# Kernel tuning notes

Hardware: AMD Instinct MI355X
Metric: run time of the kernel (lower is better)

## Reference

```python
import jax, jax.numpy as jnp
import numpy as np

B, N, M, T, D, NH = 64, 1024, 32, 8, 512, 8
OUT = 1000
NSO, NSA = N // 4, N // 8
DH = D // NH


def _conv(x, w, b):
    y = jax.lax.conv_general_dilated(x, w, (1, 1), 'SAME', dimension_numbers=('NCHW', 'OIHW', 'NCHW'))
    return y + b[None, :, None, None]


def _bn(x, g, b):
    # BatchNorm2d in train mode: per-batch statistics over (B, H, W)
    m = x.mean(axis=(0, 2, 3), keepdims=True)
    v = x.var(axis=(0, 2, 3), keepdims=True)
    return (x - m) * jax.lax.rsqrt(v + 1e-5) * g[None, :, None, None] + b[None, :, None, None]


def _mp2(x):
    b_, c, h, w = x.shape
    return x.reshape(b_, c, h // 2, 2, w // 2, 2).max(axis=(3, 5))


def _ln(x, g, b):
    m = x.mean(-1, keepdims=True)
    v = x.var(-1, keepdims=True)
    return (x - m) * jax.lax.rsqrt(v + 1e-5) * g + b


def _glu(x):
    a, b = jnp.split(x, 2, axis=-1)
    return a * jax.nn.sigmoid(b)


def setup_inputs():
    ks = iter(jax.random.split(jax.random.key(0), 64))

    def nrm(shape, fan_in):
        return jax.random.normal(next(ks), shape, jnp.float32) / np.float32(np.sqrt(fan_in))

    inp = {}
    inp['x'] = jax.random.normal(next(ks), (B, 3, 64, 64), jnp.float32)
    inp['c1w'] = nrm((16, 3, 3, 3), 27); inp['c1b'] = jnp.zeros((16,))
    inp['bn1g'] = jnp.ones((16,)); inp['bn1b'] = jnp.zeros((16,))
    inp['c2w'] = nrm((32, 16, 3, 3), 144); inp['c2b'] = jnp.zeros((32,))
    inp['bn2g'] = jnp.ones((32,)); inp['bn2b'] = jnp.zeros((32,))
    inp['c3w'] = nrm((64, 32, 3, 3), 288); inp['c3b'] = jnp.zeros((64,))
    inp['bn3g'] = jnp.ones((64,)); inp['bn3b'] = jnp.zeros((64,))
    inp['c4w'] = nrm((64, 64, 3, 3), 576); inp['c4b'] = jnp.zeros((64,))
    inp['bn4g'] = jnp.ones((64,)); inp['bn4b'] = jnp.zeros((64,))
    inp['fc1w'] = nrm((256, 256), 256); inp['fc1b'] = jnp.zeros((256,))
    inp['fc2w'] = nrm((128, D), 128); inp['fc2b'] = jnp.zeros((D,))
    inp['kvw'] = nrm((D, D), D); inp['kvb'] = jnp.zeros((D,))
    inp['kvlg'] = jnp.ones((D,)); inp['kvlb'] = jnp.zeros((D,))
    inp['synw'] = nrm((D + N, 2 * N), D + N); inp['synb'] = jnp.zeros((2 * N,))
    inp['synlg'] = jnp.ones((N,)); inp['synlb'] = jnp.zeros((N,))
    inp['nlm_w1'] = nrm((N, M, 256), M); inp['nlm_b1'] = jnp.zeros((N, 256))
    inp['nlm_w2'] = nrm((N, 128), 128); inp['nlm_b2'] = jnp.zeros((N,))
    inp['start_act'] = nrm((N,), N)
    inp['start_trace'] = nrm((N, M), N + M)
    inp['dec_a'] = jax.random.uniform(next(ks), (NSA,), jnp.float32, 0.0, 3.0)
    inp['dec_o'] = jax.random.uniform(next(ks), (NSO,), jnp.float32, 0.0, 3.0)
    inp['qw'] = nrm((NSA, D), NSA); inp['qb'] = jnp.zeros((D,))
    inp['attn_inw'] = nrm((D, 3 * D), D); inp['attn_inb'] = jnp.zeros((3 * D,))
    inp['attn_ow'] = nrm((D, D), D); inp['attn_ob'] = jnp.zeros((D,))
    inp['op_w1'] = nrm((NSO, 256), NSO); inp['op_b1'] = jnp.zeros((256,))
    inp['op_l1g'] = jnp.ones((256,)); inp['op_l1b'] = jnp.zeros((256,))
    inp['op_w2'] = nrm((256, 64), 256); inp['op_b2'] = jnp.zeros((64,))
    inp['op_l2g'] = jnp.ones((64,)); inp['op_l2b'] = jnp.zeros((64,))
    inp['op_w3'] = nrm((64, OUT), 64); inp['op_b3'] = jnp.zeros((OUT,))
    inp['aL'] = jax.random.randint(next(ks), (NSA,), 0, N)
    inp['aR'] = jax.random.randint(next(ks), (NSA,), 0, N)
    inp['oL'] = jax.random.randint(next(ks), (NSO,), 0, N)
    inp['oR'] = jax.random.randint(next(ks), (NSO,), 0, N)
    inp['task_idx'] = 0
    return inp


def _forward(x, c1w, c1b, bn1g, bn1b, c2w, c2b, bn2g, bn2b, c3w, c3b, bn3g, bn3b, c4w, c4b, bn4g, bn4b, fc1w, fc1b, fc2w, fc2b, kvw, kvb, kvlg, kvlb, synw, synb, synlg, synlb, nlm_w1, nlm_b1, nlm_w2, nlm_b2, start_act, start_trace, dec_a, dec_o, qw, qb, attn_inw, attn_inb, attn_ow, attn_ob, op_w1, op_b1, op_l1g, op_l1b, op_w2, op_b2, op_l2g, op_l2b, op_w3, op_b3, aL, aR, oL, oR):
    # --- AdaptiveCNNEncoder (3-channel branch) ---
    h = jax.nn.relu(_bn(_conv(x, c1w, c1b), bn1g, bn1b))
    h = jax.nn.relu(_bn(_conv(h, c2w, c2b), bn2g, bn2b))
    h = _mp2(h)
    h = jax.nn.relu(_bn(_conv(h, c3w, c3b), bn3g, bn3b))
    h = _mp2(h)
    h = jax.nn.relu(_bn(_conv(h, c4w, c4b), bn4g, bn4b))
    b_, c, hh, ww = h.shape
    # AdaptiveAvgPool2d((2,2)): mean over equal blocks (16x16 -> 2x2)
    h = h.reshape(b_, c, 2, hh // 2, 2, ww // 2).mean(axis=(3, 5)).reshape(b_, c * 4)
    enc = _glu(h @ fc1w + fc1b) @ fc2w + fc2b            # (B, D)
    kv = _ln(enc @ kvw + kvb, kvlg, kvlb)                # single kv token

    Wq, Wk, Wv = jnp.split(attn_inw, 3, axis=1)
    bq, bk, bv = jnp.split(attn_inb, 3)
    kh = (kv @ Wk + bk).reshape(B, NH, DH)
    vh = (kv @ Wv + bv).reshape(B, NH, DH)

    r_a = jnp.exp(-jnp.clip(dec_a, 0.0, 15.0))           # (NSA,)
    r_o = jnp.exp(-jnp.clip(dec_o, 0.0, 15.0))           # (NSO,)

    act0 = jnp.broadcast_to(start_act, (B, N))
    trace0 = jnp.broadcast_to(start_trace, (B, N, M))
    ao0 = act0[:, oL] * act0[:, oR]                      # initial out-sync accumulators
    bo0 = jnp.ones_like(ao0)
    inv_log_out = np.float32(1.0 / np.log(OUT))
    inv_sqrt_dh = np.float32(1.0 / np.sqrt(DH))

    def tick(carry, t):
        act, trace, aa, ba, ao, bo = carry
        pp = act[:, aL] * act[:, aR]
        first = (t == 0)
        aa = jnp.where(first, pp, r_a * aa + pp)
        ba = jnp.where(first, jnp.ones_like(ba), r_a * ba + 1.0)
        sync_a = aa * jax.lax.rsqrt(ba + 1e-8)
        qv = sync_a @ qw + qb
        qh = (qv @ Wq + bq).reshape(B, NH, DH)
        logits = jnp.einsum('bhd,bhd->bh', qh, kh) * inv_sqrt_dh
        w = jax.nn.softmax(logits[..., None], axis=-1)[..., 0]  # single key -> ones
        attn_out = (w[..., None] * vh).reshape(B, D) @ attn_ow + attn_ob
        pre = jnp.concatenate([attn_out, act], axis=-1)
        state = _ln(_glu(pre @ synw + synb), synlg, synlb)
        trace = jnp.concatenate([trace[:, :, 1:], state[:, :, None]], axis=-1)
        # per-neuron private MLPs, batched: (B,N,M)x(N,M,256) -> GLU -> (N,128) -> scalar
        hid = _glu(jnp.einsum('bnm,nmh->bnh', trace, nlm_w1) + nlm_b1)
        act = jnp.einsum('bnh,nh->bn', hid, nlm_w2) + nlm_b2
        po = act[:, oL] * act[:, oR]
        ao = r_o * ao + po
        bo = r_o * bo + 1.0
        sync_o = ao * jax.lax.rsqrt(bo + 1e-8)
        h1 = jax.nn.relu(_ln(sync_o @ op_w1 + op_b1, op_l1g, op_l1b))
        h2 = jax.nn.relu(_ln(h1 @ op_w2 + op_b2, op_l2g, op_l2b))
        pred = h2 @ op_w3 + op_b3
        p = jax.nn.softmax(pred, axis=-1)
        ent = -jnp.sum(p * jnp.log(p + 1e-10), axis=-1)
        ne = ent * inv_log_out
        cert = jnp.stack([ne, 1.0 - ne], axis=-1)
        return (act, trace, aa, ba, ao, bo), (pred, cert)

    carry0 = (act0, trace0, jnp.zeros((B, NSA), jnp.float32), jnp.zeros((B, NSA), jnp.float32), ao0, bo0)
    _, (preds, certs) = jax.lax.scan(tick, carry0, jnp.arange(T))
    return jnp.transpose(preds, (1, 2, 0)), jnp.transpose(certs, (1, 2, 0))


def reference(x, c1w, c1b, bn1g, bn1b, c2w, c2b, bn2g, bn2b, c3w, c3b, bn3g, bn3b, c4w, c4b, bn4g, bn4b, fc1w, fc1b, fc2w, fc2b, kvw, kvb, kvlg, kvlb, synw, synb, synlg, synlb, nlm_w1, nlm_b1, nlm_w2, nlm_b2, start_act, start_trace, dec_a, dec_o, qw, qb, attn_inw, attn_inb, attn_ow, attn_ob, op_w1, op_b1, op_l1g, op_l1b, op_w2, op_b2, op_l2g, op_l2b, op_w3, op_b3, aL, aR, oL, oR, task_idx):
    del task_idx  # single task; all task-indexed params are for task 0
    return _forward(x, c1w, c1b, bn1g, bn1b, c2w, c2b, bn2g, bn2b, c3w, c3b, bn3g, bn3b, c4w, c4b, bn4g, bn4b, fc1w, fc1b, fc2w, fc2b, kvw, kvb, kvlg, kvlb, synw, synb, synlg, synlb, nlm_w1, nlm_b1, nlm_w2, nlm_b2, start_act, start_trace, dec_a, dec_o, qw, qb, attn_inw, attn_inb, attn_ow, attn_ob, op_w1, op_b1, op_l1g, op_l1b, op_w2, op_b2, op_l2g, op_l2b, op_w3, op_b3, aL, aR, oL, oR)
```

## Files before the change

kernel.cpp:

```cpp
#include <hip/hip_runtime.h>
#include <math.h>

constexpr int B_ = 64, N_ = 1024, M_ = 32, T_ = 8;
constexpr int OUT_ = 1000, NSO_ = 256;

#define DEVFN __device__ __forceinline__

typedef __attribute__((ext_vector_type(8))) short bf16x8;
typedef __attribute__((ext_vector_type(4))) float f32x4;

DEVFN float blockReduceSum(float v, float* buf) {
  int t = threadIdx.x;
  buf[t] = v; __syncthreads();
  for (int off = blockDim.x >> 1; off > 0; off >>= 1) {
    if (t < off) buf[t] += buf[t + off];
    __syncthreads();
  }
  float r = buf[0];
  __syncthreads();
  return r;
}

DEVFN float sigmoidf_(float x) { return 1.f / (1.f + __expf(-x)); }

DEVFN unsigned short f2bf(float f) {
  unsigned u = __float_as_uint(f);
  unsigned r = (u + 0x7FFFu + ((u >> 16) & 1u)) >> 16;
  return (unsigned short)r;
}
DEVFN float bf2f(unsigned short h) { return __uint_as_float((unsigned)h << 16); }

template<int NW>
DEVFN float bsum(float v, float* red) {
  #pragma unroll
  for (int o = 32; o > 0; o >>= 1) v += __shfl_xor(v, o);
  int w = threadIdx.x >> 6, ln = threadIdx.x & 63;
  if (ln == 0) red[w] = v;
  __syncthreads();
  if (w == 0) {
    float x = (ln < NW) ? red[ln] : 0.f;
    #pragma unroll
    for (int o = 8; o > 0; o >>= 1) x += __shfl_xor(x, o);
    if (ln == 0) red[0] = x;
  }
  __syncthreads();
  float r = red[0];
  __syncthreads();
  return r;
}

template<int NW>
DEVFN float bmax(float v, float* red) {
  #pragma unroll
  for (int o = 32; o > 0; o >>= 1) v = fmaxf(v, __shfl_xor(v, o));
  int w = threadIdx.x >> 6, ln = threadIdx.x & 63;
  if (ln == 0) red[w] = v;
  __syncthreads();
  if (w == 0) {
    float x = (ln < NW) ? red[ln] : -INFINITY;
    #pragma unroll
    for (int o = 8; o > 0; o >>= 1) x = fmaxf(x, __shfl_xor(x, o));
    if (ln == 0) red[0] = x;
  }
  __syncthreads();
  float r = red[0];
  __syncthreads();
  return r;
}

DEVFN void bn_ssl(float2* ssl, const float* bnpart, const float* g, const float* bb,
                  int C, int ns, float inv_n) {
  for (int c = threadIdx.x; c < C; c += blockDim.x) {
    float s1 = 0.f, s2 = 0.f;
    for (int s = 0; s < ns; ++s) { s1 += bnpart[(c * ns + s) * 2]; s2 += bnpart[(c * ns + s) * 2 + 1]; }
    float m = s1 * inv_n;
    float var = s2 * inv_n - m * m;
    float rstd = rsqrtf(var + 1e-5f);
    float sc = g[c] * rstd;
    ssl[c] = make_float2(sc, bb[c] - m * sc);
  }
}

__global__ __launch_bounds__(256)
void k_wprep(const float* __restrict__ c2w, const float* __restrict__ c3w,
             const float* __restrict__ c4w, unsigned short* __restrict__ wt2,
             unsigned short* __restrict__ wt3, unsigned short* __restrict__ wt4) {
  int i = blockIdx.x * 256 + threadIdx.x;
  if (i < 5120) {
    int tap = i / 512, co = (i / 16) % 32, ci = i & 15;
    wt2[i] = (tap < 9) ? f2bf(c2w[(co * 16 + ci) * 9 + tap]) : 0;
  } else if (i < 5120 + 18432) {
    int j = i - 5120;
    int tap = j / 2048, co = (j / 32) % 64, ci = j & 31;
    wt3[j] = f2bf(c3w[(co * 32 + ci) * 9 + tap]);
  } else if (i < 5120 + 18432 + 36864) {
    int j = i - 5120 - 18432;
    int tap = j / 4096, co = (j / 64) % 64, ci = j & 63;
    wt4[j] = f2bf(c4w[(co * 64 + ci) * 9 + tap]);
  }
}

__global__ __launch_bounds__(256)
void k_w1t(const float* __restrict__ w1, unsigned short* __restrict__ w1t) {
  int n = blockIdx.x;
  __shared__ float tile[32][260];
  const float* src = w1 + (size_t)n * 8192;
  for (int i = threadIdx.x; i < 8192; i += 256)
    tile[i >> 8][i & 255] = src[i];
  __syncthreads();
  int c = threadIdx.x;
  unsigned short* dst = w1t + ((size_t)n * 256 + c) * 32;
  #pragma unroll
  for (int q = 0; q < 8; ++q) {
    ushort4 o;
    o.x = f2bf(tile[q * 4 + 0][c]); o.y = f2bf(tile[q * 4 + 1][c]);
    o.z = f2bf(tile[q * 4 + 2][c]); o.w = f2bf(tile[q * 4 + 3][c]);
    *reinterpret_cast<ushort4*>(dst + q * 4) = o;
  }
}

__global__ __launch_bounds__(256)
void k_synwt(const float* __restrict__ synw2, unsigned short* __restrict__ Bt) {
  int j0 = blockIdx.x * 64, k0 = blockIdx.y * 64;
  __shared__ float tile[64][65];
  for (int i = threadIdx.x; i < 4096; i += 256) {
    int kk = i >> 6, jj = i & 63;
    tile[kk][jj] = synw2[(size_t)(k0 + kk) * 2048 + j0 + jj];
  }
  __syncthreads();
  int jj = threadIdx.x >> 2, kq = (threadIdx.x & 3) * 16;
  unsigned short* dst = Bt + (size_t)(j0 + jj) * 1024 + k0 + kq;
  #pragma unroll
  for (int q = 0; q < 4; ++q) {
    ushort4 o;
    o.x = f2bf(tile[kq + q * 4 + 0][jj]); o.y = f2bf(tile[kq + q * 4 + 1][jj]);
    o.z = f2bf(tile[kq + q * 4 + 2][jj]); o.w = f2bf(tile[kq + q * 4 + 3][jj]);
    *reinterpret_cast<ushort4*>(dst + q * 4) = o;
  }
}

__global__ __launch_bounds__(256)
void k_conv1(const float* __restrict__ in, const float* __restrict__ wgl,
             unsigned short* __restrict__ outp) {
  constexpr int HW = 64, TY = 4, XV = 4, XQ = 16, CPT = 4;
  __shared__ __align__(16) float ins[3][TY + 2][HW + 8];
  const int b = blockIdx.x, y0 = blockIdx.y * TY, tid = threadIdx.x;
  const int sp = tid & 63;
  const int cg = __builtin_amdgcn_readfirstlane(tid >> 6);
  const int xq = sp % XQ, yr = sp / XQ, x0 = xq * XV;
  float acc[CPT][XV];
  #pragma unroll
  for (int j = 0; j < CPT; ++j)
    #pragma unroll
    for (int k = 0; k < XV; ++k) acc[j][k] = 0.f;
  constexpr int NEL = 3 * (TY + 2) * (HW + 8);
  for (int i = tid; i < NEL; i += 256) {
    int col = i % (HW + 8), row = (i / (HW + 8)) % (TY + 2), ci = i / ((HW + 8) * (TY + 2));
    int gx = col - 4, gy = y0 + row - 1;
    float v = 0.f;
    if (gx >= 0 && gx < HW && gy >= 0 && gy < HW)
      v = in[((size_t)(b * 3 + ci) * HW + gy) * HW + gx];
    ins[ci][row][col] = v;
  }
  __syncthreads();
  for (int ci = 0; ci < 3; ++ci) {
    const float* wci = wgl + ((size_t)(cg * CPT) * 3 + ci) * 9;
    #pragma unroll
    for (int dy = 0; dy < 3; ++dy) {
      const float* r = &ins[ci][yr + dy][x0 + 4];
      float win[6];
      win[0] = r[-1];
      float4 m = *reinterpret_cast<const float4*>(r);
      win[1] = m.x; win[2] = m.y; win[3] = m.z; win[4] = m.w;
      win[5] = r[4];
      #pragma unroll
      for (int j = 0; j < CPT; ++j) {
        const float* wj = wci + (size_t)j * 27 + dy * 3;
        float w0 = wj[0], w1 = wj[1], w2 = wj[2];
        #pragma unroll
        for (int k = 0; k < XV; ++k)
          acc[j][k] = fmaf(win[k], w0, fmaf(win[k + 1], w1, fmaf(win[k + 2], w2, acc[j][k])));
      }
    }
  }
  #pragma unroll
  for (int j = 0; j < CPT; ++j) {
    unsigned short* op = outp + (((size_t)b * 16 + cg * CPT + j) * HW + y0 + yr) * HW + x0;
    ushort4 o;
    o.x = f2bf(acc[j][0]); o.y = f2bf(acc[j][1]); o.z = f2bf(acc[j][2]); o.w = f2bf(acc[j][3]);
    *reinterpret_cast<ushort4*>(op) = o;
  }
}

__global__ __launch_bounds__(256)
void k_conv2_mfma(const unsigned short* __restrict__ in, const unsigned short* __restrict__ wt2,
                  const float* __restrict__ bnpart, const float* __restrict__ bng,
                  const float* __restrict__ bnb, unsigned short* __restrict__ outp) {
  const int b = blockIdx.x, y = blockIdx.y;
  const int tid = threadIdx.x;
  const int w = tid >> 6, lane = tid & 63;
  const int col = lane & 15, kg = lane >> 4;
  const int p0 = w * 16;
  __shared__ unsigned short lds[3][68][16];
  __shared__ float2 ssl[16];
  bn_ssl(ssl, bnpart, bng, bnb, 16, 32, 1.f / (float)(B_ * 4096));
  __syncthreads();
  for (int i = tid; i < 3 * 66 * 16; i += 256) {
    int px = i % 66, row = (i / 66) % 3, ci = i / 198;
    int gy = y + row - 1, gx = px - 1;
    float v = 0.f;
    if (gy >= 0 && gy < 64 && gx >= 0 && gx < 64) {
      float2 s = ssl[ci];
      v = fmaxf(fmaf(bf2f(in[((size_t)(b * 16 + ci) * 64 + gy) * 64 + gx]), s.x, s.y), 0.f);
    }
    lds[row][px][ci] = f2bf(v);
  }
  __syncthreads();
  f32x4 acc0 = {0.f, 0.f, 0.f, 0.f}, acc1 = {0.f, 0.f, 0.f, 0.f};
  const int tsel = kg >> 1, ci0 = (kg & 1) * 8;
  #pragma unroll
  for (int p = 0; p < 5; ++p) {
    int tap = 2 * p + tsel;
    int dy = (tap < 9) ? tap / 3 : 0;
    int dx = (tap < 9) ? tap % 3 : 0;
    bf16x8 af = *reinterpret_cast<const bf16x8*>(&lds[dy][p0 + col + dx][ci0]);
    bf16x8 b0 = *reinterpret_cast<const bf16x8*>(wt2 + ((size_t)tap * 32 + col) * 16 + ci0);
    bf16x8 b1 = *reinterpret_cast<const bf16x8*>(wt2 + ((size_t)tap * 32 + 16 + col) * 16 + ci0);
    acc0 = __builtin_amdgcn_mfma_f32_16x16x32_bf16(af, b0, acc0, 0, 0, 0);
    acc1 = __builtin_amdgcn_mfma_f32_16x16x32_bf16(af, b1, acc1, 0, 0, 0);
  }
  int px = p0 + kg * 4;
  ushort4 o0, o1;
  o0.x = f2bf(acc0[0]); o0.y = f2bf(acc0[1]); o0.z = f2bf(acc0[2]); o0.w = f2bf(acc0[3]);
  o1.x = f2bf(acc1[0]); o1.y = f2bf(acc1[1]); o1.z = f2bf(acc1[2]); o1.w = f2bf(acc1[3]);
  *reinterpret_cast<ushort4*>(outp + ((size_t)(b * 32 + col) * 64 + y) * 64 + px) = o0;
  *reinterpret_cast<ushort4*>(outp + ((size_t)(b * 32 + 16 + col) * 64 + y) * 64 + px) = o1;
}

__global__ __launch_bounds__(256)
void k_conv3_mfma(const unsigned short* __restrict__ in, const unsigned short* __restrict__ wt3,
                  const float* __restrict__ bnpart, const float* __restrict__ bng,
                  const float* __restrict__ bnb, unsigned short* __restrict__ outp) {
  const int b = blockIdx.x, y0 = blockIdx.y * 2;
  const int tid = threadIdx.x;
  const int w = tid >> 6, lane = tid & 63;
  const int col = lane & 15, kg = lane >> 4;
  const int yloc = w >> 1, p0 = (w & 1) * 16;
  __shared__ unsigned short lds[4][34][40];
  __shared__ float2 ssl[32];
  bn_ssl(ssl, bnpart, bng, bnb, 32, 32, 1.f / (float)(B_ * 4096));
  __syncthreads();
  for (int i = tid; i < 4 * 34 * 32; i += 256) {
    int px = i % 34, row = (i / 34) % 4, ci = i / 136;
    int gy = y0 + row - 1, gx = px - 1;
    float v = 0.f;
    if (gy >= 0 && gy < 32 && gx >= 0 && gx < 32) {
      float2 s = ssl[ci];
      size_t base = ((size_t)(b * 32 + ci) * 64 + 2 * gy) * 64 + 2 * gx;
      float r0 = fmaf(bf2f(in[base]),      s.x, s.y);
      float r1 = fmaf(bf2f(in[base + 1]),  s.x, s.y);
      float r2 = fmaf(bf2f(in[base + 64]), s.x, s.y);
      float r3 = fmaf(bf2f(in[base + 65]), s.x, s.y);
      v = fmaxf(fmaxf(fmaxf(r0, r1), fmaxf(r2, r3)), 0.f);
    }
    lds[row][px][ci] = f2bf(v);
  }
  __syncthreads();
  f32x4 acc[4];
  #pragma unroll
  for (int c = 0; c < 4; ++c) acc[c] = (f32x4){0.f, 0.f, 0.f, 0.f};
  #pragma unroll
  for (int tap = 0; tap < 9; ++tap) {
    int dy = tap / 3, dx = tap % 3;
    bf16x8 af = *reinterpret_cast<const bf16x8*>(&lds[yloc + dy][p0 + col + dx][kg * 8]);
    #pragma unroll
    for (int c = 0; c < 4; ++c) {
      bf16x8 bfr = *reinterpret_cast<const bf16x8*>(wt3 + ((size_t)tap * 64 + c * 16 + col) * 32 + kg * 8);
      acc[c] = __builtin_amdgcn_mfma_f32_16x16x32_bf16(af, bfr, acc[c], 0, 0, 0);
    }
  }
  int yy = y0 + yloc, px = p0 + kg * 4;
  #pragma unroll
  for (int c = 0; c < 4; ++c) {
    ushort4 o;
    o.x = f2bf(acc[c][0]); o.y = f2bf(acc[c][1]); o.z = f2bf(acc[c][2]); o.w = f2bf(acc[c][3]);
    *reinterpret_cast<ushort4*>(outp + ((size_t)(b * 64 + c * 16 + col) * 32 + yy) * 32 + px) = o;
  }
}

__global__ __launch_bounds__(128)
void k_conv4_mfma(const unsigned short* __restrict__ in, const unsigned short* __restrict__ wt4,
                  const float* __restrict__ bnpart, const float* __restrict__ bng,
                  const float* __restrict__ bnb, unsigned short* __restrict__ outp) {
  const int b = blockIdx.x, y0 = blockIdx.y * 2;
  const int tid = threadIdx.x;
  const int w = tid >> 6, lane = tid & 63;
  const int col = lane & 15, kg = lane >> 4;
  __shared__ unsigned short lds[4][18][72];
  __shared__ float2 ssl[64];
  bn_ssl(ssl, bnpart, bng, bnb, 64, 16, 1.f / (float)(B_ * 1024));
  __syncthreads();
  for (int i = tid; i < 4 * 18 * 64; i += 128) {
    int px = i % 18, row = (i / 18) % 4, ci = i / 72;
    int gy = y0 + row - 1, gx = px - 1;
    float v = 0.f;
    if (gy >= 0 && gy < 16 && gx >= 0 && gx < 16) {
      float2 s = ssl[ci];
      size_t base = ((size_t)(b * 64 + ci) * 32 + 2 * gy) * 32 + 2 * gx;
      float r0 = fmaf(bf2f(in[base]),      s.x, s.y);
      float r1 = fmaf(bf2f(in[base + 1]),  s.x, s.y);
      float r2 = fmaf(bf2f(in[base + 32]), s.x, s.y);
      float r3 = fmaf(bf2f(in[base + 33]), s.x, s.y);
      v = fmaxf(fmaxf(fmaxf(r0, r1), fmaxf(r2, r3)), 0.f);
    }
    lds[row][px][ci] = f2bf(v);
  }
  __syncthreads();
  f32x4 acc[4];
  #pragma unroll
  for (int c = 0; c < 4; ++c) acc[c] = (f32x4){0.f, 0.f, 0.f, 0.f};
  #pragma unroll
  for (int tap = 0; tap < 9; ++tap) {
    int dy = tap / 3, dx = tap % 3;
    #pragma unroll
    for (int kc = 0; kc < 2; ++kc) {
      bf16x8 af = *reinterpret_cast<const bf16x8*>(&lds[w + dy][col + dx][kc * 32 + kg * 8]);
      #pragma unroll
      for (int c = 0; c < 4; ++c) {
        bf16x8 bfr = *reinterpret_cast<const bf16x8*>(wt4 + ((size_t)tap * 64 + c * 16 + col) * 64 + kc * 32 + kg * 8);
        acc[c] = __builtin_amdgcn_mfma_f32_16x16x32_bf16(af, bfr, acc[c], 0, 0, 0);
      }
    }
  }
  int yy = y0 + w, px = kg * 4;
  #pragma unroll
  for (int c = 0; c < 4; ++c) {
    ushort4 o;
    o.x = f2bf(acc[c][0]); o.y = f2bf(acc[c][1]); o.z = f2bf(acc[c][2]); o.w = f2bf(acc[c][3]);
    *reinterpret_cast<ushort4*>(outp + ((size_t)(b * 64 + c * 16 + col) * 16 + yy) * 16 + px) = o;
  }
}

template<int C, int HW2>
__global__ __launch_bounds__(256)
void k_bn_stats_bf(const unsigned short* __restrict__ x, float* __restrict__ part) {
  int c = blockIdx.x, s = blockIdx.y, ns = gridDim.y;
  const int Np2 = B_ * HW2 / 2;
  float s1 = 0.f, s2 = 0.f;
  for (int ii = s * 256 + threadIdx.x; ii < Np2; ii += ns * 256) {
    int b = ii / (HW2 / 2), p2 = ii % (HW2 / 2);
    const unsigned short* pp = x + ((size_t)b * C + c) * HW2 + p2 * 2;
    unsigned u = *reinterpret_cast<const unsigned*>(pp);
    float v0 = __uint_as_float(u << 16);
    float v1 = __uint_as_float(u & 0xFFFF0000u);
    s1 += v0 + v1; s2 += v0 * v0 + v1 * v1;
  }
  __shared__ float r1[256], r2[256];
  r1[threadIdx.x] = s1; r2[threadIdx.x] = s2; __syncthreads();
  for (int off = 128; off > 0; off >>= 1) {
    if (threadIdx.x < off) { r1[threadIdx.x] += r1[threadIdx.x + off]; r2[threadIdx.x] += r2[threadIdx.x + off]; }
    __syncthreads();
  }
  if (threadIdx.x == 0) {
    part[(c * ns + s) * 2 + 0] = r1[0];
    part[(c * ns + s) * 2 + 1] = r2[0];
  }
}

__global__ __launch_bounds__(256)
void k_avgpool_bn_bf(const unsigned short* __restrict__ x, const float* __restrict__ bnpart,
                     const float* __restrict__ g, const float* __restrict__ bb,
                     float* __restrict__ outp) {
  __shared__ float2 ssl[64];
  bn_ssl(ssl, bnpart, g, bb, 64, 8, 1.f / (float)(B_ * 256));
  __syncthreads();
  int idx = blockIdx.x * 256 + threadIdx.x;
  int b = idx >> 8;
  int r = idx & 255;
  int c = r >> 2, i = (r >> 1) & 1, j = r & 1;
  float2 s = ssl[c];
  const unsigned short* p = x + ((size_t)(b * 64 + c) * 16 + i * 8) * 16 + j * 8;
  float sum = 0.f;
  #pragma unroll
  for (int yy = 0; yy < 8; ++yy)
    #pragma unroll
    for (int xx = 0; xx < 8; ++xx)
      sum += fmaxf(fmaf(bf2f(p[yy * 16 + xx]), s.x, s.y), 0.f);
  outp[idx] = sum * (1.f / 64.f);
}

template<int K, int NOUT>
__global__ __launch_bounds__(256)
void k_gemm_part(const float* __restrict__ A, const float* __restrict__ W, int ldw,
                 float* __restrict__ part) {
  int jt = blockIdx.x, ks = blockIdx.y;
  int k0 = ks * 64;
  __shared__ float As[64][65];
  for (int i = threadIdx.x; i < 4096; i += 256) {
    int r = i >> 6, c = i & 63;
    As[r][c] = A[(size_t)r * K + k0 + c];
  }
  __syncthreads();
  int jsub = threadIdx.x & 31;
  int bg = threadIdx.x >> 5;
  int j = jt * 32 + jsub;
  float acc[8] = {0.f, 0.f, 0.f, 0.f, 0.f, 0.f, 0.f, 0.f};
  const float* wp = W + (size_t)k0 * ldw + j;
  #pragma unroll 8
  for (int kk = 0; kk < 64; ++kk) {
    float w = wp[(size_t)kk * ldw];
    #pragma unroll
    for (int r = 0; r < 8; ++r) acc[r] = fmaf(As[bg * 8 + r][kk], w, acc[r]);
  }
  float* pp = part + (size_t)ks * 64 * NOUT + j;
  #pragma unroll
  for (int r = 0; r < 8; ++r) pp[(size_t)(bg * 8 + r) * NOUT] = acc[r];
}

template<int NOUT, int NO_FIN, int KS, bool GLU_, bool LN_>
__global__ __launch_bounds__(256)
void k_fc_reduce(const float* __restrict__ part, const float* __restrict__ bias, int bstride,
                 const float* __restrict__ lng, const float* __restrict__ lnb,
                 float* __restrict__ outp) {
  constexpr int R = (NO_FIN + 255) / 256;
  int b = blockIdx.x, t = threadIdx.x;
  const float* bp = bias + (size_t)b * bstride;
  float v[R];
  #pragma unroll
  for (int r = 0; r < R; ++r) {
    int j = t + r * 256;
    if (j < NO_FIN) {
      float za = bp[j];
      float zb = GLU_ ? bp[j + NO_FIN] : 0.f;
      #pragma unroll
      for (int ks = 0; ks < KS; ++ks) {
        const float* pr = part + ((size_t)ks * 64 + b) * NOUT;
        za += pr[j];
        if (GLU_) zb += pr[j + NO_FIN];
      }
      v[r] = GLU_ ? za * sigmoidf_(zb) : za;
    } else v[r] = 0.f;
  }
  if (LN_) {
    __shared__ float red[256];
    float s1 = 0.f, s2 = 0.f;
    #pragma unroll
    for (int r = 0; r < R; ++r) { s1 += v[r]; s2 += v[r] * v[r]; }
    s1 = blockReduceSum(s1, red);
    s2 = blockReduceSum(s2, red);
    float mu = s1 / (float)NO_FIN;
    float rstd = rsqrtf(s2 / (float)NO_FIN - mu * mu + 1e-5f);
    #pragma unroll
    for (int r = 0; r < R; ++r) {
      int j = t + r * 256;
      if (j < NO_FIN) outp[(size_t)b * NO_FIN + j] = fmaf((v[r] - mu) * rstd, lng[j], lnb[j]);
    }
  } else {
    #pragma unroll
    for (int r = 0; r < R; ++r) {
      int j = t + r * 256;
      if (j < NO_FIN) outp[(size_t)b * NO_FIN + j] = v[r];
    }
  }
}

__global__ __launch_bounds__(256)
void k_syn_mfma(const unsigned short* __restrict__ Abf, const unsigned short* __restrict__ Bt,
                float* __restrict__ part) {
  const int jt = blockIdx.x, ks = blockIdx.y;
  const int w = threadIdx.x >> 6, lane = threadIdx.x & 63;
  const int col = lane & 15, kg = lane >> 4;
  const int jcol = jt * 64 + w * 16 + col;
  const int k0 = ks * 256;
  f32x4 acc[4];
  #pragma unroll
  for (int mt = 0; mt < 4; ++mt) acc[mt] = (f32x4){0.f, 0.f, 0.f, 0.f};
  #pragma unroll
  for (int kb = 0; kb < 8; ++kb) {
    const int kk = k0 + kb * 32 + kg * 8;
    bf16x8 bfr = *reinterpret_cast<const bf16x8*>(Bt + (size_t)jcol * 1024 + kk);
    #pragma unroll
    for (int mt = 0; mt < 4; ++mt) {
      bf16x8 a = *reinterpret_cast<const bf16x8*>(Abf + (size_t)(mt * 16 + col) * 1024 + kk);
      acc[mt] = __builtin_amdgcn_mfma_f32_16x16x32_bf16(a, bfr, acc[mt], 0, 0, 0);
    }
  }
  #pragma unroll
  for (int mt = 0; mt < 4; ++mt) {
    int b0 = mt * 16 + kg * 4;
    #pragma unroll
    for (int r = 0; r < 4; ++r)
      part[((size_t)ks * 64 + b0 + r) * 2048 + jcol] = acc[mt][r];
  }
}

__global__ __launch_bounds__(1024)
void k_syn_reduce(const float* __restrict__ part, const float* __restrict__ syncst,
                  const float* __restrict__ g, const float* __restrict__ bb,
                  unsigned short* __restrict__ trace, int slot) {
  int b = blockIdx.x, t = threadIdx.x;
  __shared__ float red[16];
  float za = syncst[b * 2048 + t];
  float zb = syncst[b * 2048 + 1024 + t];
  #pragma unroll
  for (int ks = 0; ks < 4; ++ks) {
    const float* pr = part + ((size_t)ks * 64 + b) * 2048;
    za += pr[t];
    zb += pr[t + 1024];
  }
  float v = za * sigmoidf_(zb);
  float s1 = bsum<16>(v, red);
  float s2 = bsum<16>(v * v, red);
  float mu = s1 * (1.f / 1024.f);
  float rstd = rsqrtf(s2 * (1.f / 1024.f) - mu * mu + 1e-5f);
  trace[((size_t)t * 64 + b) * 32 + slot] = f2bf(fmaf((v - mu) * rstd, g[t], bb[t]));
}

__global__ __launch_bounds__(256)
void k_init(const float* __restrict__ sa, const float* __restrict__ st,
            const int* __restrict__ oL, const int* __restrict__ oR,
            float* __restrict__ act, unsigned short* __restrict__ act_bf,
            unsigned short* __restrict__ trace,
            float* __restrict__ ao, float* __restrict__ bo) {
  int idx = blockIdx.x * 256 + threadIdx.x;
  if (idx < B_ * N_ * M_) {
    int n = idx >> 11, m = idx & 31;
    trace[idx] = f2bf(st[n * 32 + m]);
  }
  if (idx < B_ * N_) {
    float v = sa[idx % N_];
    act[idx] = v;
    act_bf[idx] = f2bf(v);
  }
  if (idx < B_ * NSO_) {
    int i = idx % NSO_;
    ao[idx] = sa[oL[i]] * sa[oR[i]];
    bo[idx] = 1.f;
  }
}

__global__ __launch_bounds__(128)
void k_nlm_mfma(const unsigned short* __restrict__ trace, const unsigned short* __restrict__ w1t,
                const float* __restrict__ b1, const float* __restrict__ w2,
                const float* __restrict__ b2, float* __restrict__ act,
                unsigned short* __restrict__ act_bf, int tick) {
  const int w = threadIdx.x >> 6, lane = threadIdx.x & 63;
  const int n = blockIdx.x * 2 + w;
  const int col = lane & 15, kg = lane >> 4;
  __shared__ __align__(16) unsigned short ldsA[2][64][40];
  {
    const uint4* src = reinterpret_cast<const uint4*>(trace + ((size_t)n * 64 + lane) * 32);
    uint4 r0 = src[0], r1 = src[1], r2 = src[2], r3 = src[3];
    uint4* d = reinterpret_cast<uint4*>(&ldsA[w][lane][0]);
    d[0] = r0; d[1] = r1; d[2] = r2; d[3] = r3;
  }
  bf16x8 bf[16];
  float b1v[16], w2v[8];
  #pragma unroll
  for (int nt = 0; nt < 16; ++nt) {
    bf[nt] = *reinterpret_cast<const bf16x8*>(w1t + (((size_t)n * 256 + nt * 16 + col) * 32 + kg * 8));
    b1v[nt] = b1[n * 256 + nt * 16 + col];
  }
  #pragma unroll
  for (int nt = 0; nt < 8; ++nt) w2v[nt] = w2[n * 128 + nt * 16 + col];
  const float b2n = b2[n];
  const int kbase = kg * 8 + ((tick + 1) & 31);
  __syncthreads();
  #pragma unroll
  for (int mt = 0; mt < 4; ++mt) {
    const int brow = mt * 16 + col;
    bf16x8 af;
    #pragma unroll
    for (int j = 0; j < 8; ++j)
      af[j] = (short)ldsA[w][brow][(kbase + j) & 31];
    f32x4 acc[16];
    #pragma unroll
    for (int nt = 0; nt < 16; ++nt)
      acc[nt] = __builtin_amdgcn_mfma_f32_16x16x32_bf16(af, bf[nt], (f32x4){0.f, 0.f, 0.f, 0.f}, 0, 0, 0);
    float v0 = 0.f, v1 = 0.f, v2 = 0.f, v3 = 0.f;
    #pragma unroll
    for (int nt = 0; nt < 8; ++nt) {
      f32x4 za = acc[nt], zb = acc[nt + 8];
      float ba = b1v[nt], bg = b1v[nt + 8], wv = w2v[nt];
      v0 = fmaf((za[0] + ba) * sigmoidf_(zb[0] + bg), wv, v0);
      v1 = fmaf((za[1] + ba) * sigmoidf_(zb[1] + bg), wv, v1);
      v2 = fmaf((za[2] + ba) * sigmoidf_(zb[2] + bg), wv, v2);
      v3 = fmaf((za[3] + ba) * sigmoidf_(zb[3] + bg), wv, v3);
    }
    #pragma unroll
    for (int o = 1; o <= 8; o <<= 1) {
      v0 += __shfl_xor(v0, o); v1 += __shfl_xor(v1, o);
      v2 += __shfl_xor(v2, o); v3 += __shfl_xor(v3, o);
    }
    if (col == 0) {
      int b0 = mt * 16 + kg * 4;
      float r0 = v0 + b2n, r1 = v1 + b2n, r2 = v2 + b2n, r3 = v3 + b2n;
      act[(size_t)(b0 + 0) * 1024 + n] = r0;
      act[(size_t)(b0 + 1) * 1024 + n] = r1;
      act[(size_t)(b0 + 2) * 1024 + n] = r2;
      act[(size_t)(b0 + 3) * 1024 + n] = r3;
      act_bf[(size_t)(b0 + 0) * 1024 + n] = f2bf(r0);
      act_bf[(size_t)(b0 + 1) * 1024 + n] = f2bf(r1);
      act_bf[(size_t)(b0 + 2) * 1024 + n] = f2bf(r2);
      act_bf[(size_t)(b0 + 3) * 1024 + n] = f2bf(r3);
    }
  }
}

__global__ __launch_bounds__(1024)
void k_outpath(const float* __restrict__ act, float* __restrict__ ao, float* __restrict__ bo,
               const float* __restrict__ dec_o, const int* __restrict__ oL, const int* __restrict__ oR,
               const float* __restrict__ opw1, const float* __restrict__ opb1,
               const float* __restrict__ l1g, const float* __restrict__ l1b,
               const float* __restrict__ opw2, const float* __restrict__ opb2,
               const float* __restrict__ l2g, const float* __restrict__ l2b,
               const float* __restrict__ opw3, const float* __restrict__ opb3,
               float* __restrict__ outp, int tick) {
  int b = blockIdx.x, t = threadIdx.x;
  __shared__ float red[16];
  __shared__ float syo[256], h1s[256], h2s[64];
  __shared__ float zp1[4][256];
  __shared__ float zp2[16][64];
  const float* actb = act + (size_t)b * 1024;
  if (t < 256) {
    float po = actb[oL[t]] * actb[oR[t]];
    float r = __expf(-fminf(fmaxf(dec_o[t], 0.f), 15.f));
    int ai = b * 256 + t;
    float av = fmaf(r, ao[ai], po);
    float bv = fmaf(r, bo[ai], 1.f);
    ao[ai] = av; bo[ai] = bv;
    syo[t] = av * rsqrtf(bv + 1e-8f);
  }
  __syncthreads();
  {
    int j = t & 255, ks = t >> 8;
    float z = 0.f;
    const float* wcol = opw1 + j;
    #pragma unroll 8
    for (int k = ks * 64; k < ks * 64 + 64; ++k) z = fmaf(syo[k], wcol[k * 256], z);
    zp1[ks][j] = z;
  }
  __syncthreads();
  float h1v = 0.f;
  if (t < 256) h1v = zp1[0][t] + zp1[1][t] + zp1[2][t] + zp1[3][t] + opb1[t];
  float s1 = bsum<16>(t < 256 ? h1v : 0.f, red);
  float s2 = bsum<16>(t < 256 ? h1v * h1v : 0.f, red);
  if (t < 256) {
    float mu = s1 * (1.f / 256.f);
    float rstd = rsqrtf(s2 * (1.f / 256.f) - mu * mu + 1e-5f);
    h1s[t] = fmaxf(fmaf((h1v - mu) * rstd, l1g[t], l1b[t]), 0.f);
  }
  __syncthreads();
  {
    int j = t & 63, ks = t >> 6;
    float z = 0.f;
    const float* wcol = opw2 + j;
    #pragma unroll
    for (int k = ks * 16; k < ks * 16 + 16; ++k) z = fmaf(h1s[k], wcol[k * 64], z);
    zp2[ks][j] = z;
  }
  __syncthreads();
  if (t < 64) {
    float z2 = opb2[t];
    #pragma unroll
    for (int ks = 0; ks < 16; ++ks) z2 += zp2[ks][t];
    float a1 = z2, a2 = z2 * z2;
    #pragma unroll
    for (int o = 32; o > 0; o >>= 1) { a1 += __shfl_xor(a1, o); a2 += __shfl_xor(a2, o); }
    float mu2 = a1 * (1.f / 64.f);
    float rs2 = rsqrtf(a2 * (1.f / 64.f) - mu2 * mu2 + 1e-5f);
    h2s[t] = fmaxf(fmaf((z2 - mu2) * rs2, l2g[t], l2b[t]), 0.f);
  }
  __syncthreads();
  float z3 = 0.f;
  if (t < OUT_) {
    z3 = opb3[t];
    const float* wcol = opw3 + t;
    #pragma unroll 8
    for (int k = 0; k < 64; ++k) z3 = fmaf(h2s[k], wcol[k * OUT_], z3);
    outp[(size_t)b * (OUT_ * T_) + (size_t)t * T_ + tick] = z3;
  }
  float mx = bmax<16>(t < OUT_ ? z3 : -INFINITY, red);
  float e = (t < OUT_) ? __expf(z3 - mx) : 0.f;
  float S = bsum<16>(e, red);
  float inv = 1.f / S;
  float ep = 0.f;
  if (t < OUT_) {
    float p = e * inv;
    ep = p * __logf(p + 1e-10f);
  }
  float ent = -bsum<16>(ep, red);
  if (t == 0) {
    float ne = ent * (1.f / logf(1000.f));
    outp[(size_t)B_ * OUT_ * T_ + (size_t)b * 2 * T_ + tick]      = ne;
    outp[(size_t)B_ * OUT_ * T_ + (size_t)b * 2 * T_ + T_ + tick] = 1.f - ne;
  }
}

extern "C" void kernel_launch(void* const* d_in, const int* in_sizes, int n_in,
                              void* d_out, int out_size, void* d_ws, size_t ws_size,
                              hipStream_t stream) {
  (void)in_sizes; (void)n_in; (void)out_size; (void)ws_size;
  const float* x      = (const float*)d_in[0];
  const float* c1w    = (const float*)d_in[1];
  const float* bn1g   = (const float*)d_in[3];
  const float* bn1b   = (const float*)d_in[4];
  const float* c2w    = (const float*)d_in[5];
  const float* bn2g   = (const float*)d_in[7];
  const float* bn2b   = (const float*)d_in[8];
  const float* c3w    = (const float*)d_in[9];
  const float* bn3g   = (const float*)d_in[11];
  const float* bn3b   = (const float*)d_in[12];
  const float* c4w    = (const float*)d_in[13];
  const float* bn4g   = (const float*)d_in[15];
  const float* bn4b   = (const float*)d_in[16];
  const float* fc1w   = (const float*)d_in[17];
  const float* fc1b   = (const float*)d_in[18];
  const float* fc2w   = (const float*)d_in[19];
  const float* fc2b   = (const float*)d_in[20];
  const float* kvw    = (const float*)d_in[21];
  const float* kvb    = (const float*)d_in[22];
  const float* kvlg   = (const float*)d_in[23];
  const float* kvlb   = (const float*)d_in[24];
  const float* synw   = (const float*)d_in[25];
  const float* synb   = (const float*)d_in[26];
  const float* synlg  = (const float*)d_in[27];
  const float* synlb  = (const float*)d_in[28];
  const float* nlmw1  = (const float*)d_in[29];
  const float* nlmb1  = (const float*)d_in[30];
  const float* nlmw2  = (const float*)d_in[31];
  const float* nlmb2  = (const float*)d_in[32];
  const float* sact   = (const float*)d_in[33];
  const float* strc   = (const float*)d_in[34];
  const float* dec_o  = (const float*)d_in[36];
  const float* attn_inw = (const float*)d_in[39];
  const float* attn_inb = (const float*)d_in[40];
  const float* attn_ow  = (const float*)d_in[41];
  const float* attn_ob  = (const float*)d_in[42];
  const float* opw1   = (const float*)d_in[43];
  const float* opb1   = (const float*)d_in[44];
  const float* opl1g  = (const float*)d_in[45];
  const float* opl1b  = (const float*)d_in[46];
  const float* opw2   = (const float*)d_in[47];
  const float* opb2   = (const float*)d_in[48];
  const float* opl2g  = (const float*)d_in[49];
  const float* opl2b  = (const float*)d_in[50];
  const float* opw3   = (const float*)d_in[51];
  const float* opb3   = (const float*)d_in[52];
  const int*   oL     = (const int*)d_in[55];
  const int*   oR     = (const int*)d_in[56];
  float* outp = (float*)d_out;
  float* ws   = (float*)d_ws;

  unsigned short* c1raw_bf = (unsigned short*)(ws + 8388608);
  unsigned short* c2raw_bf = (unsigned short*)ws;
  unsigned short* c3raw_bf = (unsigned short*)(ws + 8388608);
  unsigned short* c4raw_bf = (unsigned short*)ws;
  float* part  = ws + 4194304;
  unsigned short* trace_bf = (unsigned short*)(ws + 6291456);
  float* act   = ws + 8388608;
  float* syncst= ws + 8454144;
  float* pooled= ws + 8585216;
  float* ench  = ws + 8601600;
  float* enc   = ws + 8609792;
  float* kvbuf = ws + 8642560;
  float* vhbuf = ws + 8675328;
  float* aout  = ws + 8708096;
  float* ao    = ws + 8740864;
  float* bo    = ws + 8757248;
  unsigned short* w1t_bf   = (unsigned short*)(ws + 8777728);
  unsigned short* synw2t_bf= (unsigned short*)(ws + 12972032);
  unsigned short* wt2 = (unsigned short*)(ws + 14061568);
  unsigned short* wt3 = (unsigned short*)(ws + 14064128);
  unsigned short* wt4 = (unsigned short*)(ws + 14073344);
  float* bnpart = ws + 14091776;
  unsigned short* act_bf = (unsigned short*)(ws + 14095872);

  k_wprep<<<236,256,0,stream>>>(c2w, c3w, c4w, wt2, wt3, wt4);

  k_conv1<<<dim3(64,16),256,0,stream>>>(x, c1w, c1raw_bf);
  k_bn_stats_bf<16,4096><<<dim3(16,32),256,0,stream>>>(c1raw_bf, bnpart);

  k_conv2_mfma<<<dim3(64,64),256,0,stream>>>(c1raw_bf, wt2, bnpart, bn1g, bn1b, c2raw_bf);
  k_bn_stats_bf<32,4096><<<dim3(32,32),256,0,stream>>>(c2raw_bf, bnpart);

  k_conv3_mfma<<<dim3(64,16),256,0,stream>>>(c2raw_bf, wt3, bnpart, bn2g, bn2b, c3raw_bf);
  k_bn_stats_bf<64,1024><<<dim3(64,16),256,0,stream>>>(c3raw_bf, bnpart);

  k_conv4_mfma<<<dim3(64,8),128,0,stream>>>(c3raw_bf, wt4, bnpart, bn3g, bn3b, c4raw_bf);

  k_w1t<<<1024,256,0,stream>>>(nlmw1, w1t_bf);
  k_synwt<<<dim3(32,16),256,0,stream>>>(synw + (size_t)512 * 2048, synw2t_bf);

  k_bn_stats_bf<64,256><<<dim3(64,8),256,0,stream>>>(c4raw_bf, bnpart);
  k_avgpool_bn_bf<<<64,256,0,stream>>>(c4raw_bf, bnpart, bn4g, bn4b, pooled);

  k_gemm_part<256,256><<<dim3(8,4),256,0,stream>>>(pooled, fc1w, 256, part);
  k_fc_reduce<256,128,4,true,false><<<64,256,0,stream>>>(part, fc1b, 0, nullptr, nullptr, ench);
  k_gemm_part<128,512><<<dim3(16,2),256,0,stream>>>(ench, fc2w, 512, part);
  k_fc_reduce<512,512,2,false,false><<<64,256,0,stream>>>(part, fc2b, 0, nullptr, nullptr, enc);
  k_gemm_part<512,512><<<dim3(16,8),256,0,stream>>>(enc, kvw, 512, part);
  k_fc_reduce<512,512,8,false,true><<<64,256,0,stream>>>(part, kvb, 0, kvlg, kvlb, kvbuf);
  k_gemm_part<512,512><<<dim3(16,8),256,0,stream>>>(kvbuf, attn_inw + 1024, 1536, part);
  k_fc_reduce<512,512,8,false,false><<<64,256,0,stream>>>(part, attn_inb + 1024, 0, nullptr, nullptr, vhbuf);
  k_gemm_part<512,512><<<dim3(16,8),256,0,stream>>>(vhbuf, attn_ow, 512, part);
  k_fc_reduce<512,512,8,false,false><<<64,256,0,stream>>>(part, attn_ob, 0, nullptr, nullptr, aout);
  k_gemm_part<512,2048><<<dim3(64,8),256,0,stream>>>(aout, synw, 2048, part);
  k_fc_reduce<2048,2048,8,false,false><<<64,256,0,stream>>>(part, synb, 0, nullptr, nullptr, syncst);

  k_init<<<8192,256,0,stream>>>(sact, strc, oL, oR, act, act_bf, trace_bf, ao, bo);

  for (int t = 0; t < T_; ++t) {
    k_syn_mfma<<<dim3(32,4),256,0,stream>>>(act_bf, synw2t_bf, part);
    k_syn_reduce<<<64,1024,0,stream>>>(part, syncst, synlg, synlb, trace_bf, t);
    k_nlm_mfma<<<512,128,0,stream>>>(trace_bf, w1t_bf, nlmb1, nlmw2, nlmb2, act, act_bf, t);
    k_outpath<<<64,1024,0,stream>>>(act, ao, bo, dec_o, oL, oR,
                                    opw1, opb1, opl1g, opl1b,
                                    opw2, opb2, opl2g, opl2b,
                                    opw3, opb3, outp, t);
  }
}
```

Measured before the change: 526.5 us.

## Fuse synapse reduce into GEMM epilogue and defer LayerNorm to NLM kernel

Removes the split-K partial buffer and the separate synapse reduce kernel. Each GEMM block now covers the full K=1024 for 32 paired neurons, applies the GLU with the synch bias in its epilogue, and writes per-block partial sums for the LayerNorm statistics. The NLM kernel then finishes those statistics, normalises its own neuron value, and writes it into the trace before running its MFMA. This drops one launch and one round trip through global memory per tick. In exchange the GEMM grid shrinks from 128 blocks to 32 with a four-times-longer K loop, and every NLM block redundantly re-reduces the 32 partial sums.

```diff
diff --git a/kernel.cpp b/kernel.cpp
--- a/kernel.cpp
+++ b/kernel.cpp
@@ -465,19 +465,22 @@
 }
 
 __global__ __launch_bounds__(256)
-void k_syn_mfma(const unsigned short* __restrict__ Abf, const unsigned short* __restrict__ Bt,
-                float* __restrict__ part) {
-  const int jt = blockIdx.x, ks = blockIdx.y;
+void k_syn_mfma2(const unsigned short* __restrict__ Abf, const unsigned short* __restrict__ Bt,
+                 const float* __restrict__ syncst, float* __restrict__ vout,
+                 float* __restrict__ part2f) {
+  __shared__ float zsh[2][32][64];
+  __shared__ float vsh[32][64];
   const int w = threadIdx.x >> 6, lane = threadIdx.x & 63;
   const int col = lane & 15, kg = lane >> 4;
-  const int jcol = jt * 64 + w * 16 + col;
-  const int k0 = ks * 256;
+  const int hi = w >> 1;
+  const int nl = (w & 1) * 16 + col;
+  const int jcol = hi * 1024 + blockIdx.x * 32 + nl;
   f32x4 acc[4];
   #pragma unroll
   for (int mt = 0; mt < 4; ++mt) acc[mt] = (f32x4){0.f, 0.f, 0.f, 0.f};
-  #pragma unroll
-  for (int kb = 0; kb < 8; ++kb) {
-    const int kk = k0 + kb * 32 + kg * 8;
+  #pragma unroll 4
+  for (int kb = 0; kb < 32; ++kb) {
+    const int kk = kb * 32 + kg * 8;
     bf16x8 bfr = *reinterpret_cast<const bf16x8*>(Bt + (size_t)jcol * 1024 + kk);
     #pragma unroll
     for (int mt = 0; mt < 4; ++mt) {
@@ -490,30 +493,29 @@
     int b0 = mt * 16 + kg * 4;
     #pragma unroll
     for (int r = 0; r < 4; ++r)
-      part[((size_t)ks * 64 + b0 + r) * 2048 + jcol] = acc[mt][r];
-  }
-}
-
-__global__ __launch_bounds__(1024)
-void k_syn_reduce(const float* __restrict__ part, const float* __restrict__ syncst,
-                  const float* __restrict__ g, const float* __restrict__ bb,
-                  unsigned short* __restrict__ trace, int slot) {
-  int b = blockIdx.x, t = threadIdx.x;
-  __shared__ float red[16];
-  float za = syncst[b * 2048 + t];
-  float zb = syncst[b * 2048 + 1024 + t];
-  #pragma unroll
-  for (int ks = 0; ks < 4; ++ks) {
-    const float* pr = part + ((size_t)ks * 64 + b) * 2048;
-    za += pr[t];
-    zb += pr[t + 1024];
-  }
-  float v = za * sigmoidf_(zb);
-  float s1 = bsum<16>(v, red);
-  float s2 = bsum<16>(v * v, red);
-  float mu = s1 * (1.f / 1024.f);
-  float rstd = rsqrtf(s2 * (1.f / 1024.f) - mu * mu + 1e-5f);
-  trace[((size_t)t * 64 + b) * 32 + slot] = f2bf(fmaf((v - mu) * rstd, g[t], bb[t]));
+      zsh[hi][nl][b0 + r] = acc[mt][r];
+  }
+  __syncthreads();
+  #pragma unroll
+  for (int q = 0; q < 8; ++q) {
+    int idx = threadIdx.x + q * 256;
+    int nloc = idx >> 6, b = idx & 63;
+    int n = blockIdx.x * 32 + nloc;
+    float za = zsh[0][nloc][b] + syncst[b * 2048 + n];
+    float zb = zsh[1][nloc][b] + syncst[b * 2048 + 1024 + n];
+    float v = za * sigmoidf_(zb);
+    vout[n * 64 + b] = v;
+    vsh[nloc][b] = v;
+  }
+  __syncthreads();
+  if (threadIdx.x < 64) {
+    int b = threadIdx.x;
+    float s1 = 0.f, s2 = 0.f;
+    #pragma unroll
+    for (int i = 0; i < 32; ++i) { float v = vsh[i][b]; s1 += v; s2 += v * v; }
+    float2* p2 = reinterpret_cast<float2*>(part2f);
+    p2[b * 32 + blockIdx.x] = make_float2(s1, s2);
+  }
 }
 
 __global__ __launch_bounds__(256)
@@ -540,7 +542,9 @@
 }
 
 __global__ __launch_bounds__(128)
-void k_nlm_mfma(const unsigned short* __restrict__ trace, const unsigned short* __restrict__ w1t,
+void k_nlm_mfma(unsigned short* __restrict__ trace, const unsigned short* __restrict__ w1t,
+                const float* __restrict__ vout, const float* __restrict__ part2f,
+                const float* __restrict__ lng, const float* __restrict__ lnb,
                 const float* __restrict__ b1, const float* __restrict__ w2,
                 const float* __restrict__ b2, float* __restrict__ act,
                 unsigned short* __restrict__ act_bf, int tick) {
@@ -549,10 +553,20 @@
   const int col = lane & 15, kg = lane >> 4;
   __shared__ __align__(16) unsigned short ldsA[2][64][40];
   {
+    const float2* p2 = reinterpret_cast<const float2*>(part2f);
+    float s1 = 0.f, s2 = 0.f;
+    #pragma unroll
+    for (int i = 0; i < 32; ++i) { float2 pv = p2[lane * 32 + i]; s1 += pv.x; s2 += pv.y; }
+    float mu = s1 * (1.f / 1024.f);
+    float rstd = rsqrtf(s2 * (1.f / 1024.f) - mu * mu + 1e-5f);
+    float vv = vout[n * 64 + lane];
+    unsigned short vbf = f2bf(fmaf((vv - mu) * rstd, lng[n], lnb[n]));
     const uint4* src = reinterpret_cast<const uint4*>(trace + ((size_t)n * 64 + lane) * 32);
     uint4 r0 = src[0], r1 = src[1], r2 = src[2], r3 = src[3];
     uint4* d = reinterpret_cast<uint4*>(&ldsA[w][lane][0]);
     d[0] = r0; d[1] = r1; d[2] = r2; d[3] = r3;
+    ldsA[w][lane][tick] = vbf;
+    trace[((size_t)n * 64 + lane) * 32 + tick] = vbf;
   }
   bf16x8 bf[16];
   float b1v[16], w2v[8];
@@ -757,6 +771,8 @@
   unsigned short* c3raw_bf = (unsigned short*)(ws + 8388608);
   unsigned short* c4raw_bf = (unsigned short*)ws;
   float* part  = ws + 4194304;
+  float* vout  = ws + 4194304;
+  float* part2f= ws + 4259840;
   unsigned short* trace_bf = (unsigned short*)(ws + 6291456);
   float* act   = ws + 8388608;
   float* syncst= ws + 8454144;
@@ -811,9 +827,9 @@
   k_init<<<8192,256,0,stream>>>(sact, strc, oL, oR, act, act_bf, trace_bf, ao, bo);
 
   for (int t = 0; t < T_; ++t) {
-    k_syn_mfma<<<dim3(32,4),256,0,stream>>>(act_bf, synw2t_bf, part);
-    k_syn_reduce<<<64,1024,0,stream>>>(part, syncst, synlg, synlb, trace_bf, t);
-    k_nlm_mfma<<<512,128,0,stream>>>(trace_bf, w1t_bf, nlmb1, nlmw2, nlmb2, act, act_bf, t);
+    k_syn_mfma2<<<32,256,0,stream>>>(act_bf, synw2t_bf, syncst, vout, part2f);
+    k_nlm_mfma<<<512,128,0,stream>>>(trace_bf, w1t_bf, vout, part2f, synlg, synlb,
+                                     nlmb1, nlmw2, nlmb2, act, act_bf, t);
     k_outpath<<<64,1024,0,stream>>>(act, ao, bo, dec_o, oL, oR,
                                     opw1, opb1, opl1g, opl1b,
                                     opw2, opb2, opl2g, opl2b,
```

Result: slower. 631.6 us (+19.9%).
